# Kernel tuning notes

Measured on AMD Instinct MI355X. Metric: run time of the kernel, lower is better.

The kernel has to match this reference:

```python
import jax, jax.numpy as jnp
import numpy as np

N, DM, F, G, FG = 4096, 512, 128, 8, 16
DH, DE, ES = 128, 256, 4
E = G * ES
GROUP_TOP_K, EXPERT_TOP_K = 2, 2
TEMP = 1.0
LN_EPS = 1e-5


def _ln(x, g, b):
    m = jnp.mean(x, axis=-1, keepdims=True)
    v = jnp.mean((x - m) ** 2, axis=-1, keepdims=True)
    return (x - m) * jax.lax.rsqrt(v + LN_EPS) * g + b


def _topk_softmax(logits, k):
    # faithful to torch _topk_softmax: softmax over top-k values, zeros elsewhere
    vals, idx = jax.lax.top_k(logits, k)
    w = jax.nn.softmax(vals, axis=-1)
    oh = jax.nn.one_hot(idx, logits.shape[-1], dtype=logits.dtype)  # [..., k, E]
    return jnp.einsum('...ke,...k->...e', oh, w)


def setup_inputs() -> dict:
    key = jax.random.key(0)
    ks = iter(jax.random.split(key, 32))
    n = lambda shape, s=0.02: jax.random.normal(next(ks), shape, dtype=jnp.float32) * s
    d = {
        'hidden': jax.random.normal(next(ks), (N, DM), dtype=jnp.float32),
        'feat': jax.random.normal(next(ks), (N, F), dtype=jnp.float32),
        # pre_ln
        'pre_ln_g': jnp.ones((DM,), jnp.float32), 'pre_ln_b': jnp.zeros((DM,), jnp.float32),
        # router_hidden_encoder: LN(DM) -> Lin(DM,DH) -> GELU -> Lin(DH,DH)
        'rh_ln_g': jnp.ones((DM,), jnp.float32), 'rh_ln_b': jnp.zeros((DM,), jnp.float32),
        'rh_w1': n((DM, DH)), 'rh_b1': jnp.zeros((DH,), jnp.float32),
        'rh_w2': n((DH, DH)), 'rh_b2': jnp.zeros((DH,), jnp.float32),
        # stage_feature_encoder: LN(F) -> Lin(F,DH) -> GELU -> Lin(DH,DH)
        'sf_ln_g': jnp.ones((F,), jnp.float32), 'sf_ln_b': jnp.zeros((F,), jnp.float32),
        'sf_w1': n((F, DH)), 'sf_b1': jnp.zeros((DH,), jnp.float32),
        'sf_w2': n((DH, DH)), 'sf_b2': jnp.zeros((DH,), jnp.float32),
        # group_feature_encoders (stacked over G): LN(FG) -> Lin(FG,DH) -> GELU -> Lin(DH,DH)
        'gf_ln_g': jnp.ones((G, FG), jnp.float32), 'gf_ln_b': jnp.zeros((G, FG), jnp.float32),
        'gf_w1': n((G, FG, DH)), 'gf_b1': jnp.zeros((G, DH), jnp.float32),
        'gf_w2': n((G, DH, DH)), 'gf_b2': jnp.zeros((G, DH), jnp.float32),
        # per_group_scorer (ScalarRouter): Lin(4DH,DH) -> GELU -> Lin(DH,1)
        'pgs_w1': n((4 * DH, DH)), 'pgs_b1': jnp.zeros((DH,), jnp.float32),
        'pgs_w2': n((DH,)), 'pgs_b2': jnp.zeros((), jnp.float32),
        # intra_routers (stacked over G): Lin(4DH,DH) -> GELU -> Lin(DH,ES)
        'ir_w1': n((G, 4 * DH, DH)), 'ir_b1': jnp.zeros((G, DH), jnp.float32),
        'ir_w2': n((G, DH, ES)), 'ir_b2': jnp.zeros((G, ES), jnp.float32),
        # experts (stacked over E = G*ES, group-major): Lin(DM,DE) -> GELU -> Lin(DE,DM)
        'ex_w1': n((E, DM, DE)), 'ex_b1': jnp.zeros((E, DE), jnp.float32),
        'ex_w2': n((E, DE, DM)), 'ex_b2': jnp.zeros((E, DM), jnp.float32),
    }
    return d


def reference(hidden, feat, pre_ln_g, pre_ln_b, rh_ln_g, rh_ln_b, rh_w1, rh_b1, rh_w2, rh_b2,
              sf_ln_g, sf_ln_b, sf_w1, sf_b1, sf_w2, sf_b2,
              gf_ln_g, gf_ln_b, gf_w1, gf_b1, gf_w2, gf_b2,
              pgs_w1, pgs_b1, pgs_w2, pgs_b2,
              ir_w1, ir_b1, ir_w2, ir_b2,
              ex_w1, ex_b1, ex_w2, ex_b2):
    # expert input (pre-LN hidden)
    h_norm = _ln(hidden, pre_ln_g, pre_ln_b)                         # [N, DM]

    # factorized router encoders
    h_enc = jax.nn.gelu(_ln(hidden, rh_ln_g, rh_ln_b) @ rh_w1 + rh_b1) @ rh_w2 + rh_b2   # [N, DH]
    s_enc = jax.nn.gelu(_ln(feat, sf_ln_g, sf_ln_b) @ sf_w1 + sf_b1) @ sf_w2 + sf_b2     # [N, DH]
    gfeat = feat.reshape(N, G, FG)                                    # disjoint contiguous group features
    g_h = jax.nn.gelu(jnp.einsum('ngf,gfh->ngh', _ln(gfeat, gf_ln_g, gf_ln_b), gf_w1) + gf_b1)
    g_enc = jnp.einsum('ngh,ghk->ngk', g_h, gf_w2) + gf_b2            # [N, G, DH]

    hB = jnp.broadcast_to(h_enc[:, None, :], (N, G, DH))
    sB = jnp.broadcast_to(s_enc[:, None, :], (N, G, DH))
    router_in = jnp.concatenate([hB, sB, g_enc, hB * g_enc], axis=-1)  # [N, G, 4DH]

    # per-group scalar scores -> group logits -> top-k scatter softmax
    pg_h = jax.nn.gelu(jnp.einsum('ngi,ih->ngh', router_in, pgs_w1) + pgs_b1)
    group_logits = (jnp.einsum('ngh,h->ng', pg_h, pgs_w2) + pgs_b2) / max(TEMP, 1e-6)    # [N, G]
    group_w = _topk_softmax(group_logits, GROUP_TOP_K)                 # [N, G]

    # intra-group expert routers -> top-k scatter softmax over expert_scale
    ir_h = jax.nn.gelu(jnp.einsum('ngi,gih->ngh', router_in, ir_w1) + ir_b1)
    intra_logits = jnp.einsum('ngh,ghe->nge', ir_h, ir_w2) + ir_b2     # [N, G, ES]
    intra_w = _topk_softmax(intra_logits, EXPERT_TOP_K)                # [N, G, ES]

    comb_w = (group_w[:, :, None] * intra_w).reshape(N, E)             # group-major expert order

    # per-expert GELU MLPs on pre-LN hidden (dense compute, sparse weights)
    eh = jax.nn.gelu(jnp.einsum('nd,edh->neh', h_norm, ex_w1) + ex_b1) # [N, E, DE]
    eo = jnp.einsum('neh,ehd->ned', eh, ex_w2) + ex_b2                 # [N, E, DM]
    out = jnp.einsum('ne,ned->nd', comb_w, eo)                         # [N, DM]
    return out
```

## Files before the change

### kernel.cpp

```cpp
#include <hip/hip_runtime.h>
#include <hip/hip_bf16.h>
#include <math.h>

#define N_TOK 4096
#define DM 512
#define FDIM 128
#define G 8
#define FG 16
#define DH 128
#define DE 256
#define ES 4
#define E_EXP 32
#define LN_EPS 1e-5f
#define BT 32

typedef __attribute__((ext_vector_type(8))) short bf16x8;
typedef __attribute__((ext_vector_type(4))) float f32x4;

#define MFMA16(a, b, c) __builtin_amdgcn_mfma_f32_16x16x32_bf16((a), (b), (c), 0, 0, 0)

#define PSTRIDE 6144

__device__ __forceinline__ float gelu_t(float x) {
    const float c = 0.7978845608028654f;
    float x3 = x * x * x;
    return 0.5f * x * (1.0f + tanhf(c * (x + 0.044715f * x3)));
}

__device__ __forceinline__ short f2bf(float f) {
    __hip_bfloat16 h = __float2bfloat16(f);
    return *reinterpret_cast<short*>(&h);
}
__device__ __forceinline__ float bf2f(short s) {
    __hip_bfloat16 h = *reinterpret_cast<__hip_bfloat16*>(&s);
    return __bfloat162float(h);
}
__device__ __forceinline__ void split3(float x, short& h, short& m, short& l) {
    h = f2bf(x);
    float r = x - bf2f(h);
    m = f2bf(r);
    float r2 = r - bf2f(m);
    l = f2bf(r2);
}

struct ConvJob { const float* src; short* dh; short* dm; short* dl;
                 int KB, NB, Kreal, plain, blk0; };
struct ConvJobs { ConvJob j[10]; };

__global__ void k_pre(ConvJobs J, int nconv,
                      const float* __restrict__ hidden,
                      const float* __restrict__ pg, const float* __restrict__ pb,
                      const float* __restrict__ rg, const float* __restrict__ rb,
                      __hip_bfloat16* __restrict__ h_normb, float* __restrict__ hL) {
    int b = blockIdx.x;
    if (b >= nconv) {
        int n = b - nconv;
        int j = threadIdx.x;
        const float* x = hidden + (size_t)n * DM;
        float v0 = x[j], v1 = x[j + 256];
        float s = v0 + v1, q = v0 * v0 + v1 * v1;
#pragma unroll
        for (int o = 32; o; o >>= 1) { s += __shfl_down(s, o); q += __shfl_down(q, o); }
        __shared__ float red[8];
        int w = j >> 6;
        if ((j & 63) == 0) { red[w] = s; red[4 + w] = q; }
        __syncthreads();
        float sum = red[0] + red[1] + red[2] + red[3];
        float sq  = red[4] + red[5] + red[6] + red[7];
        float m = sum * (1.0f / DM);
        float var = sq * (1.0f / DM) - m * m;
        float rs = rsqrtf(var + LN_EPS);
        float t0 = (v0 - m) * rs, t1 = (v1 - m) * rs;
        size_t base = (size_t)n * DM;
        h_normb[base + j]       = __float2bfloat16(t0 * pg[j]       + pb[j]);
        h_normb[base + j + 256] = __float2bfloat16(t1 * pg[j + 256] + pb[j + 256]);
        hL[base + j]           = t0 * rg[j]       + rb[j];
        hL[base + j + 256]     = t1 * rg[j + 256] + rb[j + 256];
        return;
    }
    int ji = 0;
#pragma unroll
    for (int i = 1; i < 10; i++) if (b >= J.j[i].blk0) ji = i;
    const ConvJob jb = J.j[ji];
    int rel = b - jb.blk0;
    int mat = rel / jb.KB, kb = rel % jb.KB;
    int ncols = jb.NB * 16;
    const float* s = jb.src + (size_t)mat * jb.Kreal * ncols;
    size_t dbase = ((size_t)mat * jb.KB + kb) * jb.NB * 512;
    for (int p = threadIdx.x; p < jb.NB * 64; p += 256) {
        int nb = p >> 6, lane = p & 63;
        int row0 = kb * 32 + ((lane >> 4) << 3);
        int col = nb * 16 + (lane & 15);
        if (jb.plain) {
            union { short sh[8]; uint4 v; } t;
#pragma unroll
            for (int j = 0; j < 8; j++) {
                float x = (row0 + j < jb.Kreal) ? s[(size_t)(row0 + j) * ncols + col] : 0.f;
                t.sh[j] = f2bf(x);
            }
            *(uint4*)&jb.dh[dbase + (size_t)p * 8] = t.v;
        } else {
            union { short sh[8]; uint4 v; } hi, mi, lo;
#pragma unroll
            for (int j = 0; j < 8; j++) {
                float x = (row0 + j < jb.Kreal) ? s[(size_t)(row0 + j) * ncols + col] : 0.f;
                split3(x, hi.sh[j], mi.sh[j], lo.sh[j]);
            }
            *(uint4*)&jb.dh[dbase + (size_t)p * 8] = hi.v;
            *(uint4*)&jb.dm[dbase + (size_t)p * 8] = mi.v;
            *(uint4*)&jb.dl[dbase + (size_t)p * 8] = lo.v;
        }
    }
}

__device__ __forceinline__ void emit_split_tiles(
        int tid, short (*Ah)[136], short (*Am)[136], short (*Al)[136],
        short* __restrict__ Yt, size_t panel0 ) {
    int lane_ = tid & 63, w = tid >> 6;
#pragma unroll
    for (int j = 0; j < 6; j++) {
        int combo = w * 6 + j;
        int split = combo >> 3;
        int rem = combo & 7; int t16 = rem >> 2, kb = rem & 3;
        const short* sp = (split == 0) ? &Ah[0][0] : (split == 1) ? &Am[0][0] : &Al[0][0];
        uint4 v = *(const uint4*)&sp[(t16 * 16 + (lane_ & 15)) * 136 + kb * 32 + (lane_ >> 4) * 8];
        *(uint4*)&Yt[((panel0 + t16) * 4 + kb) * 1536 + split * 512 + lane_ * 8] = v;
    }
}

template <int KB_TOT, bool DO_LN>
__device__ __forceinline__ void enc2_body(
        int bx, char* smem,
        const float* __restrict__ X,
        const float* __restrict__ lng, const float* __restrict__ lnb,
        const short* __restrict__ W1h, const short* __restrict__ W1m, const short* __restrict__ W1l,
        const float* __restrict__ B1,
        const short* __restrict__ W2h, const short* __restrict__ W2m, const short* __restrict__ W2l,
        const float* __restrict__ B2,
        short* __restrict__ Yt) {
    constexpr int K = KB_TOT * 32;
    const int n0 = bx * 32;
    const int tid = threadIdx.x;
    const int wave = tid >> 6, lane = tid & 63;
    const int quad = lane >> 4, lm = lane & 15;
    const int mt = wave & 1;
    const int ngb = (wave >> 1) * 4;

    short (*Ah)[136] = (short(*)[136])smem;
    short (*Am)[136] = (short(*)[136])(smem + 8704);
    short (*Al)[136] = (short(*)[136])(smem + 2 * 8704);

    f32x4 acc[4];
#pragma unroll
    for (int i = 0; i < 4; i++) acc[i] = (f32x4)(0.f);

    if (DO_LN) {
        for (int idx = tid; idx < 1024; idx += 256) {
            int row = idx >> 5, c4 = (idx & 31) * 4;
            float4 v = *(const float4*)&X[(size_t)(n0 + row) * K + c4];
            float s = v.x + v.y + v.z + v.w;
            float q = v.x * v.x + v.y * v.y + v.z * v.z + v.w * v.w;
#pragma unroll
            for (int o = 16; o; o >>= 1) { s += __shfl_xor(s, o); q += __shfl_xor(q, o); }
            float mean = s * (1.0f / 128.0f);
            float var = q * (1.0f / 128.0f) - mean * mean;
            float rs = rsqrtf(var + LN_EPS);
            float xv[4] = {(v.x - mean) * rs * lng[c4 + 0] + lnb[c4 + 0],
                           (v.y - mean) * rs * lng[c4 + 1] + lnb[c4 + 1],
                           (v.z - mean) * rs * lng[c4 + 2] + lnb[c4 + 2],
                           (v.w - mean) * rs * lng[c4 + 3] + lnb[c4 + 3]};
#pragma unroll
            for (int j = 0; j < 4; j++) {
                short h, m, l; split3(xv[j], h, m, l);
                Ah[row][c4 + j] = h; Am[row][c4 + j] = m; Al[row][c4 + j] = l;
            }
        }
        __syncthreads();
#pragma unroll
        for (int kb = 0; kb < KB_TOT; kb++) {
            bf16x8 ah = *(const bf16x8*)&Ah[mt * 16 + lm][kb * 32 + quad * 8];
            bf16x8 am = *(const bf16x8*)&Am[mt * 16 + lm][kb * 32 + quad * 8];
            bf16x8 al = *(const bf16x8*)&Al[mt * 16 + lm][kb * 32 + quad * 8];
#pragma unroll
            for (int nt = 0; nt < 4; nt++) {
                size_t bi = (((size_t)kb * 8 + ngb + nt) * 64 + lane) * 8;
                bf16x8 bh = *(const bf16x8*)&W1h[bi];
                bf16x8 bm = *(const bf16x8*)&W1m[bi];
                bf16x8 bl = *(const bf16x8*)&W1l[bi];
                acc[nt] = MFMA16(al, bh, acc[nt]);
                acc[nt] = MFMA16(am, bm, acc[nt]);
                acc[nt] = MFMA16(ah, bl, acc[nt]);
                acc[nt] = MFMA16(am, bh, acc[nt]);
                acc[nt] = MFMA16(ah, bm, acc[nt]);
                acc[nt] = MFMA16(ah, bh, acc[nt]);
            }
        }
    } else {
        for (int kb = 0; kb < KB_TOT; kb++) {
            const float* xs = X + (size_t)(n0 + mt * 16 + lm) * K + kb * 32 + quad * 8;
            float4 x0 = *(const float4*)xs, x1 = *(const float4*)(xs + 4);
            float xv[8] = {x0.x, x0.y, x0.z, x0.w, x1.x, x1.y, x1.z, x1.w};
            bf16x8 ah, am, al;
#pragma unroll
            for (int j = 0; j < 8; j++) {
                short h, m, l; split3(xv[j], h, m, l);
                ah[j] = h; am[j] = m; al[j] = l;
            }
#pragma unroll
            for (int nt = 0; nt < 4; nt++) {
                size_t bi = (((size_t)kb * 8 + ngb + nt) * 64 + lane) * 8;
                bf16x8 bh = *(const bf16x8*)&W1h[bi];
                bf16x8 bm = *(const bf16x8*)&W1m[bi];
                bf16x8 bl = *(const bf16x8*)&W1l[bi];
                acc[nt] = MFMA16(al, bh, acc[nt]);
                acc[nt] = MFMA16(am, bm, acc[nt]);
                acc[nt] = MFMA16(ah, bl, acc[nt]);
                acc[nt] = MFMA16(am, bh, acc[nt]);
                acc[nt] = MFMA16(ah, bm, acc[nt]);
                acc[nt] = MFMA16(ah, bh, acc[nt]);
            }
        }
    }
    __syncthreads();
#pragma unroll
    for (int nt = 0; nt < 4; nt++) {
        int col = (ngb + nt) * 16 + lm;
        float b1 = B1[col];
#pragma unroll
        for (int r = 0; r < 4; r++) {
            int row = mt * 16 + quad * 4 + r;
            short h, m, l; split3(gelu_t(acc[nt][r] + b1), h, m, l);
            Ah[row][col] = h; Am[row][col] = m; Al[row][col] = l;
        }
    }
    __syncthreads();
    f32x4 acc2[4];
#pragma unroll
    for (int i = 0; i < 4; i++) acc2[i] = (f32x4)(0.f);
#pragma unroll
    for (int kb = 0; kb < 4; kb++) {
        bf16x8 ah = *(const bf16x8*)&Ah[mt * 16 + lm][kb * 32 + quad * 8];
        bf16x8 am = *(const bf16x8*)&Am[mt * 16 + lm][kb * 32 + quad * 8];
        bf16x8 al = *(const bf16x8*)&Al[mt * 16 + lm][kb * 32 + quad * 8];
#pragma unroll
        for (int nt = 0; nt < 4; nt++) {
            size_t bi = (((size_t)kb * 8 + ngb + nt) * 64 + lane) * 8;
            bf16x8 bh = *(const bf16x8*)&W2h[bi];
            bf16x8 bm = *(const bf16x8*)&W2m[bi];
            bf16x8 bl = *(const bf16x8*)&W2l[bi];
            acc2[nt] = MFMA16(al, bh, acc2[nt]);
            acc2[nt] = MFMA16(am, bm, acc2[nt]);
            acc2[nt] = MFMA16(ah, bl, acc2[nt]);
            acc2[nt] = MFMA16(am, bh, acc2[nt]);
            acc2[nt] = MFMA16(ah, bm, acc2[nt]);
            acc2[nt] = MFMA16(ah, bh, acc2[nt]);
        }
    }
    __syncthreads();
#pragma unroll
    for (int nt = 0; nt < 4; nt++) {
        int col = (ngb + nt) * 16 + lm;
        float b2 = B2[col];
#pragma unroll
        for (int r = 0; r < 4; r++) {
            int row = mt * 16 + quad * 4 + r;
            short h, m, l; split3(acc2[nt][r] + b2, h, m, l);
            Ah[row][col] = h; Am[row][col] = m; Al[row][col] = l;
        }
    }
    __syncthreads();
    emit_split_tiles(tid, Ah, Am, Al, Yt, (size_t)bx * 2);
}

__device__ __forceinline__ void genc_one(
        int bx, int g, char* smem,
        const float* __restrict__ feat,
        const float* __restrict__ gln_g, const float* __restrict__ gln_b,
        const short* __restrict__ W1h, const short* __restrict__ W1m, const short* __restrict__ W1l,
        const float* __restrict__ gb1,
        const short* __restrict__ W2h, const short* __restrict__ W2m, const short* __restrict__ W2l,
        const float* __restrict__ gb2,
        short* __restrict__ Gs) {
    const int tid = threadIdx.x;
    const int wave = tid >> 6, lane = tid & 63;
    const int quad = lane >> 4, lm = lane & 15;
    const int mt = wave & 1;
    const int ngb = (wave >> 1) * 4;
    const int n0 = bx * 32;

    short (*Ah)[136] = (short(*)[136])smem;
    short (*Am)[136] = (short(*)[136])(smem + 8704);
    short (*Al)[136] = (short(*)[136])(smem + 2 * 8704);

    {
        int t = tid >> 3, sub = tid & 7;
        const float* fr = feat + (size_t)(n0 + t) * FDIM + g * FG;
        float xv[FG];
        float mean = 0.f;
#pragma unroll
        for (int i = 0; i < FG; i++) { xv[i] = fr[i]; mean += xv[i]; }
        mean *= (1.0f / FG);
        float var = 0.f;
#pragma unroll
        for (int i = 0; i < FG; i++) { float d = xv[i] - mean; var += d * d; }
        var *= (1.0f / FG);
        float rs = rsqrtf(var + LN_EPS);
#pragma unroll
        for (int j = 0; j < 2; j++) {
            int i = sub * 2 + j;
            float xn = (xv[i] - mean) * rs * gln_g[g * FG + i] + gln_b[g * FG + i];
            short h, m, l; split3(xn, h, m, l);
            Ah[t][i] = h; Am[t][i] = m; Al[t][i] = l;
            Ah[t][16 + i] = 0; Am[t][16 + i] = 0; Al[t][16 + i] = 0;
        }
    }
    __syncthreads();
    f32x4 acc[4];
#pragma unroll
    for (int i = 0; i < 4; i++) acc[i] = (f32x4)(0.f);
    {
        bf16x8 ah = *(const bf16x8*)&Ah[mt * 16 + lm][quad * 8];
        bf16x8 am = *(const bf16x8*)&Am[mt * 16 + lm][quad * 8];
        bf16x8 al = *(const bf16x8*)&Al[mt * 16 + lm][quad * 8];
#pragma unroll
        for (int nt = 0; nt < 4; nt++) {
            size_t bi = (((size_t)g * 8 + ngb + nt) * 64 + lane) * 8;
            bf16x8 bh = *(const bf16x8*)&W1h[bi];
            bf16x8 bm = *(const bf16x8*)&W1m[bi];
            bf16x8 bl = *(const bf16x8*)&W1l[bi];
            acc[nt] = MFMA16(al, bh, acc[nt]);
            acc[nt] = MFMA16(am, bm, acc[nt]);
            acc[nt] = MFMA16(ah, bl, acc[nt]);
            acc[nt] = MFMA16(am, bh, acc[nt]);
            acc[nt] = MFMA16(ah, bm, acc[nt]);
            acc[nt] = MFMA16(ah, bh, acc[nt]);
        }
    }
    __syncthreads();
#pragma unroll
    for (int nt = 0; nt < 4; nt++) {
        int col = (ngb + nt) * 16 + lm;
        float b1 = gb1[g * DH + col];
#pragma unroll
        for (int r = 0; r < 4; r++) {
            int row = mt * 16 + quad * 4 + r;
            short h, m, l; split3(gelu_t(acc[nt][r] + b1), h, m, l);
            Ah[row][col] = h; Am[row][col] = m; Al[row][col] = l;
        }
    }
    __syncthreads();
    f32x4 acc2[4];
#pragma unroll
    for (int i = 0; i < 4; i++) acc2[i] = (f32x4)(0.f);
#pragma unroll
    for (int kb = 0; kb < 4; kb++) {
        bf16x8 a2h = *(const bf16x8*)&Ah[mt * 16 + lm][kb * 32 + quad * 8];
        bf16x8 a2m = *(const bf16x8*)&Am[mt * 16 + lm][kb * 32 + quad * 8];
        bf16x8 a2l = *(const bf16x8*)&Al[mt * 16 + lm][kb * 32 + quad * 8];
#pragma unroll
        for (int nt = 0; nt < 4; nt++) {
            size_t bi = ((((size_t)g * 4 + kb) * 8 + ngb + nt) * 64 + lane) * 8;
            bf16x8 bh = *(const bf16x8*)&W2h[bi];
            bf16x8 bm = *(const bf16x8*)&W2m[bi];
            bf16x8 bl = *(const bf16x8*)&W2l[bi];
            acc2[nt] = MFMA16(a2l, bh, acc2[nt]);
            acc2[nt] = MFMA16(a2m, bm, acc2[nt]);
            acc2[nt] = MFMA16(a2h, bl, acc2[nt]);
            acc2[nt] = MFMA16(a2m, bh, acc2[nt]);
            acc2[nt] = MFMA16(a2h, bm, acc2[nt]);
            acc2[nt] = MFMA16(a2h, bh, acc2[nt]);
        }
    }
    __syncthreads();
#pragma unroll
    for (int nt = 0; nt < 4; nt++) {
        int col = (ngb + nt) * 16 + lm;
        float b2 = gb2[g * DH + col];
#pragma unroll
        for (int r = 0; r < 4; r++) {
            int row = mt * 16 + quad * 4 + r;
            short h, m, l; split3(acc2[nt][r] + b2, h, m, l);
            Ah[row][col] = h; Am[row][col] = m; Al[row][col] = l;
        }
    }
    __syncthreads();
    emit_split_tiles(tid, Ah, Am, Al, Gs, (size_t)g * 256 + bx * 2);
}

__global__ __launch_bounds__(256) void k_enc_all(
        const float* __restrict__ hL, const float* __restrict__ feat,
        const float* __restrict__ sf_g, const float* __restrict__ sf_b,
        const float* __restrict__ gln_g, const float* __restrict__ gln_b,
        const short* Brh1H, const short* Brh1M, const short* Brh1L, const float* rh_b1,
        const short* Brh2H, const short* Brh2M, const short* Brh2L, const float* rh_b2,
        const short* Bsf1H, const short* Bsf1M, const short* Bsf1L, const float* sf_b1,
        const short* Bsf2H, const short* Bsf2M, const short* Bsf2L, const float* sf_b2,
        const short* Bgf1H, const short* Bgf1M, const short* Bgf1L, const float* gf_b1,
        const short* Bgf2H, const short* Bgf2M, const short* Bgf2L, const float* gf_b2,
        short* __restrict__ Hs, short* __restrict__ Ss, short* __restrict__ Gs) {
    __shared__ __align__(16) char smem[3 * 8704];
    int bid = blockIdx.x;
    if (bid < 128)
        enc2_body<16, false>(bid, smem, hL, nullptr, nullptr,
                             Brh1H, Brh1M, Brh1L, rh_b1, Brh2H, Brh2M, Brh2L, rh_b2, Hs);
    else if (bid < 256)
        enc2_body<4, true>(bid - 128, smem, feat, sf_g, sf_b,
                           Bsf1H, Bsf1M, Bsf1L, sf_b1, Bsf2H, Bsf2M, Bsf2L, sf_b2, Ss);
    else {
        int idx = bid - 256;
        genc_one(idx >> 3, idx & 7, smem, feat, gln_g, gln_b,
                 Bgf1H, Bgf1M, Bgf1L, gf_b1, Bgf2H, Bgf2M, Bgf2L, gf_b2, Gs);
    }
}

__global__ __launch_bounds__(512) void k_router_mfma(
        const short* __restrict__ Hs, const short* __restrict__ Ss, const short* __restrict__ Gs,
        const short* __restrict__ BpgH, const short* __restrict__ BpgM, const short* __restrict__ BpgL,
        const short* __restrict__ BirH, const short* __restrict__ BirM, const short* __restrict__ BirL,
        const float* __restrict__ pb1, const float* __restrict__ pw2, const float* __restrict__ pb2,
        const float* __restrict__ ib1, const float* __restrict__ iw2, const float* __restrict__ ib2,
        float* __restrict__ glog, float* __restrict__ ilog) {
    const int g = blockIdx.x & 7;
    const int bx = blockIdx.x >> 3;
    const int n0 = bx * 64;
    const int tid = threadIdx.x;
    const int wave = tid >> 6, lane = tid & 63;
    const int quad = lane >> 4, lm = lane & 15;
    const bool is_pg = wave < 4;
    const int nbase = (wave & 3) * 2;
    const short* Bh = is_pg ? BpgH : (BirH + (size_t)g * 65536);
    const short* Bm = is_pg ? BpgM : (BirM + (size_t)g * 65536);
    const short* Bl = is_pg ? BpgL : (BirL + (size_t)g * 65536);

    const short* HsB = Hs + (size_t)bx * 4 * PSTRIDE;
    const short* SsB = Ss + (size_t)bx * 4 * PSTRIDE;
    const short* GsB = Gs + ((size_t)g * 256 + bx * 4) * PSTRIDE;

    __shared__ __align__(16) char smem[49152];

    int goff[6];
#pragma unroll
    for (int it = 0; it < 6; it++) {
        int lin = it * 512 + tid;
        int split = lin >> 10, rem = lin & 1023;
        int kbl = rem >> 8, t16 = (rem >> 6) & 3, ln = rem & 63;
        goff[it] = t16 * PSTRIDE + kbl * 1536 + split * 512 + ln * 8;
    }
    int roff0, roff1, woff0, woff1;
    {
        int slot = tid;
        int kbl = slot >> 8, t16 = (slot >> 6) & 3, ln = slot & 63;
        roff0 = t16 * PSTRIDE + kbl * 1536 + ln * 8;
        woff0 = kbl * 4096 + t16 * 1024 + ln * 16;
        slot = 512 + tid;
        kbl = slot >> 8; t16 = (slot >> 6) & 3; ln = slot & 63;
        roff1 = t16 * PSTRIDE + kbl * 1536 + ln * 8;
        woff1 = kbl * 4096 + t16 * 1024 + ln * 16;
    }

    f32x4 acc[4][2];
#pragma unroll
    for (int mt = 0; mt < 4; mt++)
#pragma unroll
        for (int nt = 0; nt < 2; nt++) acc[mt][nt] = (f32x4)(0.f);

    bf16x8 R[6];

#define LOADR(basep) { _Pragma("unroll") \
    for (int it = 0; it < 6; it++) R[it] = *(const bf16x8*)((basep) + goff[it]); }
#define STAGE_WRITE() { _Pragma("unroll") \
    for (int it = 0; it < 6; it++) *(bf16x8*)(smem + ((it * 512 + tid) * 16)) = R[it]; }
#define COMPUTE_CHUNK(CH) { _Pragma("unroll") \
    for (int kbl = 0; kbl < 4; kbl++) { \
        const int kb = (CH) * 4 + kbl; \
        bf16x8 Ahf[4], Amf[4], Alf[4]; \
        _Pragma("unroll") \
        for (int mt = 0; mt < 4; mt++) { \
            size_t loff = (size_t)kbl * 4096 + mt * 1024 + (size_t)lane * 16; \
            Ahf[mt] = *(const bf16x8*)(smem + loff); \
            Amf[mt] = *(const bf16x8*)(smem + 16384 + loff); \
            Alf[mt] = *(const bf16x8*)(smem + 32768 + loff); \
        } \
        _Pragma("unroll") \
        for (int nt = 0; nt < 2; nt++) { \
            size_t bi = (((size_t)kb * 8 + nbase + nt) * 64 + lane) * 8; \
            bf16x8 bh = *(const bf16x8*)&Bh[bi]; \
            bf16x8 bm = *(const bf16x8*)&Bm[bi]; \
            bf16x8 bl = *(const bf16x8*)&Bl[bi]; \
            _Pragma("unroll") \
            for (int mt = 0; mt < 4; mt++) { \
                acc[mt][nt] = MFMA16(Alf[mt], bh, acc[mt][nt]); \
                acc[mt][nt] = MFMA16(Amf[mt], bm, acc[mt][nt]); \
                acc[mt][nt] = MFMA16(Ahf[mt], bl, acc[mt][nt]); \
                acc[mt][nt] = MFMA16(Amf[mt], bh, acc[mt][nt]); \
                acc[mt][nt] = MFMA16(Ahf[mt], bm, acc[mt][nt]); \
                acc[mt][nt] = MFMA16(Ahf[mt], bh, acc[mt][nt]); \
            } \
        } \
    } }

    LOADR(HsB);
    STAGE_WRITE();
    __syncthreads();
    LOADR(SsB);
    COMPUTE_CHUNK(0);

    __syncthreads();
    STAGE_WRITE();
    __syncthreads();
    LOADR(GsB);
    COMPUTE_CHUNK(1);

    __syncthreads();
    STAGE_WRITE();
    __syncthreads();
    bf16x8 Hv0_0 = *(const bf16x8*)(HsB + roff0);
    bf16x8 Hv0_1 = *(const bf16x8*)(HsB + roff0 + 512);
    bf16x8 Hv0_2 = *(const bf16x8*)(HsB + roff0 + 1024);
    bf16x8 Gv0_0 = *(const bf16x8*)(GsB + roff0);
    bf16x8 Gv0_1 = *(const bf16x8*)(GsB + roff0 + 512);
    bf16x8 Gv0_2 = *(const bf16x8*)(GsB + roff0 + 1024);
    bf16x8 Hv1_0 = *(const bf16x8*)(HsB + roff1);
    bf16x8 Hv1_1 = *(const bf16x8*)(HsB + roff1 + 512);
    bf16x8 Hv1_2 = *(const bf16x8*)(HsB + roff1 + 1024);
    bf16x8 Gv1_0 = *(const bf16x8*)(GsB + roff1);
    bf16x8 Gv1_1 = *(const bf16x8*)(GsB + roff1 + 512);
    bf16x8 Gv1_2 = *(const bf16x8*)(GsB + roff1 + 1024);
    COMPUTE_CHUNK(2);

    bf16x8 P0h, P0m, P0l, P1h, P1m, P1l;
#pragma unroll
    for (int j = 0; j < 8; j++) {
        float hv = bf2f(Hv0_0[j]) + bf2f(Hv0_1[j]) + bf2f(Hv0_2[j]);
        float gv = bf2f(Gv0_0[j]) + bf2f(Gv0_1[j]) + bf2f(Gv0_2[j]);
        short a_, b_, c_; split3(hv * gv, a_, b_, c_);
        P0h[j] = a_; P0m[j] = b_; P0l[j] = c_;
    }
#pragma unroll
    for (int j = 0; j < 8; j++) {
        float hv = bf2f(Hv1_0[j]) + bf2f(Hv1_1[j]) + bf2f(Hv1_2[j]);
        float gv = bf2f(Gv1_0[j]) + bf2f(Gv1_1[j]) + bf2f(Gv1_2[j]);
        short a_, b_, c_; split3(hv * gv, a_, b_, c_);
        P1h[j] = a_; P1m[j] = b_; P1l[j] = c_;
    }

    __syncthreads();
    *(bf16x8*)(smem + woff0)         = P0h;
    *(bf16x8*)(smem + 16384 + woff0) = P0m;
    *(bf16x8*)(smem + 32768 + woff0) = P0l;
    *(bf16x8*)(smem + woff1)         = P1h;
    *(bf16x8*)(smem + 16384 + woff1) = P1m;
    *(bf16x8*)(smem + 32768 + woff1) = P1l;
    __syncthreads();
    COMPUTE_CHUNK(3);

#undef LOADR
#undef STAGE_WRITE
#undef COMPUTE_CHUNK

    float (*ph)[129] = (float(*)[129])smem;
    float (*ih)[129] = (float(*)[129])(smem + 32 * 129 * 4);
    for (int h = 0; h < 2; h++) {
        __syncthreads();
#pragma unroll
        for (int mi = 0; mi < 2; mi++) {
            int mt = 2 * h + mi;
#pragma unroll
            for (int nt = 0; nt < 2; nt++) {
                int col = (nbase + nt) * 16 + lm;
                float b1 = is_pg ? pb1[col] : ib1[g * DH + col];
                float* dst = is_pg ? &ph[0][0] : &ih[0][0];
#pragma unroll
                for (int r = 0; r < 4; r++) {
                    int row = mi * 16 + quad * 4 + r;
                    dst[row * 129 + col] = gelu_t(acc[mt][nt][r] + b1);
                }
            }
        }
        __syncthreads();
        if (tid < 128) {
            int t = tid >> 2, q = tid & 3;
            float s = 0.f;
            for (int i = q * 32; i < q * 32 + 32; i++) s += ph[t][i] * pw2[i];
            s += __shfl_xor(s, 1);
            s += __shfl_xor(s, 2);
            if (q == 0) glog[(size_t)(n0 + h * 32 + t) * G + g] = s + pb2[0];
        } else if (tid < 384) {
            int t2 = tid - 128;
            int t = t2 >> 3, e = (t2 >> 1) & 3, half = t2 & 1;
            const float* wv = iw2 + (size_t)g * DH * ES;
            float s = 0.f;
            for (int i = half * 64; i < half * 64 + 64; i++) s += ih[t][i] * wv[i * ES + e];
            s += __shfl_xor(s, 1);
            if (half == 0) ilog[((size_t)(n0 + h * 32 + t) * G + g) * ES + e] = s + ib2[g * ES + e];
        }
    }
}

__global__ void k_topk(const float* __restrict__ glog, const float* __restrict__ ilog,
                       int* __restrict__ cnt, int* __restrict__ toks, float* __restrict__ wgts) {
    int n = blockIdx.x * blockDim.x + threadIdx.x;
    if (n >= N_TOK) return;
    float gl[G];
#pragma unroll
    for (int g = 0; g < G; g++) gl[g] = glog[(size_t)n * G + g];
    int i1 = 0; float v1 = gl[0];
#pragma unroll
    for (int g = 1; g < G; g++) if (gl[g] > v1) { v1 = gl[g]; i1 = g; }
    int i2 = -1; float v2 = -1e30f;
#pragma unroll
    for (int g = 0; g < G; g++) if (g != i1 && gl[g] > v2) { v2 = gl[g]; i2 = g; }
    float eg = expf(v2 - v1);
    float den = 1.0f / (1.0f + eg);
    float gw_sel[2] = { den, eg * den };
    int g_sel[2] = { i1, i2 };
#pragma unroll
    for (int s = 0; s < 2; s++) {
        int g = g_sel[s]; float gw = gw_sel[s];
        float il[ES];
#pragma unroll
        for (int e = 0; e < ES; e++) il[e] = ilog[((size_t)n * G + g) * ES + e];
        int j1 = 0; float u1 = il[0];
#pragma unroll
        for (int e = 1; e < ES; e++) if (il[e] > u1) { u1 = il[e]; j1 = e; }
        int j2 = -1; float u2 = -1e30f;
#pragma unroll
        for (int e = 0; e < ES; e++) if (e != j1 && il[e] > u2) { u2 = il[e]; j2 = e; }
        float ei = expf(u2 - u1);
        float d2 = 1.0f / (1.0f + ei);
        int ex1 = g * ES + j1, ex2 = g * ES + j2;
        int p1 = atomicAdd(&cnt[ex1], 1);
        toks[(size_t)ex1 * N_TOK + p1] = n * 4 + s * 2;     wgts[(size_t)ex1 * N_TOK + p1] = gw * d2;
        int p2 = atomicAdd(&cnt[ex2], 1);
        toks[(size_t)ex2 * N_TOK + p2] = n * 4 + s * 2 + 1; wgts[(size_t)ex2 * N_TOK + p2] = gw * ei * d2;
    }
}

__global__ __launch_bounds__(512) void k_expert_mfma(
        const __hip_bfloat16* __restrict__ h_normb,
        const short* __restrict__ wB1, const float* __restrict__ eb1,
        const short* __restrict__ wB2, const float* __restrict__ eb2,
        const int* __restrict__ cnt, const int* __restrict__ toks,
        const float* __restrict__ wgts, float* __restrict__ part) {
    const int e = blockIdx.x & 31;
    const int slot = blockIdx.x >> 5;
    const int c = cnt[e];
    const int start = slot * BT;
    if (start >= c) return;
    const int m = min(BT, c - start);

    __shared__ short hs[BT][520];
    short (*es)[264] = (short(*)[264])&hs[0][0];
    __shared__ int   tok_s[BT];
    __shared__ float w_s[BT];

    const int tid = threadIdx.x;
    if (tid < BT) {
        bool ok = tid < m;
        tok_s[tid] = ok ? toks[(size_t)e * N_TOK + start + tid] : 0;
        w_s[tid]   = ok ? wgts[(size_t)e * N_TOK + start + tid] : 0.f;
    }
    __syncthreads();
    for (int idx = tid; idx < BT * 64; idx += 512) {
        int t = idx >> 6, ch = idx & 63;
        uint4 v = make_uint4(0, 0, 0, 0);
        if (t < m) v = *((const uint4*)(h_normb + (size_t)(tok_s[t] >> 2) * DM) + ch);
        *(uint4*)&hs[t][ch * 8] = v;
    }
    __syncthreads();

    const int wave = tid >> 6, lane = tid & 63;
    const int quad = lane >> 4, lm = lane & 15;

    const int ng = wave * 2;
    f32x4 acc1[2][2];
#pragma unroll
    for (int a = 0; a < 2; a++)
#pragma unroll
        for (int b = 0; b < 2; b++) acc1[a][b] = (f32x4)(0.f);
    {
        const short* w1e = wB1 + (size_t)e * DM * DE;
        for (int kb = 0; kb < 16; kb++) {
            bf16x8 a0 = *(const bf16x8*)&hs[lm][kb * 32 + quad * 8];
            bf16x8 a1 = *(const bf16x8*)&hs[16 + lm][kb * 32 + quad * 8];
            const short* wp = w1e + ((size_t)kb * 16 + ng) * 512 + lane * 8;
#pragma unroll
            for (int nt = 0; nt < 2; nt++) {
                bf16x8 b = *(const bf16x8*)(wp + nt * 512);
                acc1[0][nt] = MFMA16(a0, b, acc1[0][nt]);
                acc1[1][nt] = MFMA16(a1, b, acc1[1][nt]);
            }
        }
    }
    __syncthreads();
#pragma unroll
    for (int nt = 0; nt < 2; nt++) {
        int col = (ng + nt) * 16 + lm;
        float b1 = eb1[e * DE + col];
#pragma unroll
        for (int mt = 0; mt < 2; mt++)
#pragma unroll
        for (int r = 0; r < 4; r++) {
            int row = mt * 16 + quad * 4 + r;
            es[row][col] = f2bf(gelu_t(acc1[mt][nt][r] + b1));
        }
    }
    __syncthreads();

    {
        const int ng2 = wave * 4;
        f32x4 acc[2][4];
#pragma unroll
        for (int a = 0; a < 2; a++)
#pragma unroll
            for (int b = 0; b < 4; b++) acc[a][b] = (f32x4)(0.f);
        const short* w2e = wB2 + (size_t)e * DE * DM;
        for (int kb = 0; kb < 8; kb++) {
            bf16x8 a0 = *(const bf16x8*)&es[lm][kb * 32 + quad * 8];
            bf16x8 a1 = *(const bf16x8*)&es[16 + lm][kb * 32 + quad * 8];
            const short* wp = w2e + ((size_t)kb * 32 + ng2) * 512 + lane * 8;
#pragma unroll
            for (int nt = 0; nt < 4; nt++) {
                bf16x8 b = *(const bf16x8*)(wp + nt * 512);
                acc[0][nt] = MFMA16(a0, b, acc[0][nt]);
                acc[1][nt] = MFMA16(a1, b, acc[1][nt]);
            }
        }
        const float* b2 = eb2 + (size_t)e * DM;
#pragma unroll
        for (int mt = 0; mt < 2; mt++)
#pragma unroll
        for (int r = 0; r < 4; r++) {
            int row = mt * 16 + quad * 4 + r;
            if (row < m) {
                float w = w_s[row];
                float* prow = part + (size_t)tok_s[row] * DM;
#pragma unroll
                for (int nt = 0; nt < 4; nt++) {
                    int col = (ng2 + nt) * 16 + lm;
                    prow[col] = w * (acc[mt][nt][r] + b2[col]);
                }
            }
        }
    }
}

__global__ void k_reduce(const float* __restrict__ part, float* __restrict__ out) {
    int n = blockIdx.x;
    int j = threadIdx.x;
    const float4* p = (const float4*)(part + (size_t)n * 4 * DM);
    float4 a = p[j], b = p[128 + j], c = p[256 + j], d = p[384 + j];
    float4 r = make_float4(a.x + b.x + c.x + d.x, a.y + b.y + c.y + d.y,
                           a.z + b.z + c.z + d.z, a.w + b.w + c.w + d.w);
    ((float4*)(out + (size_t)n * DM))[j] = r;
}

extern "C" void kernel_launch(void* const* d_in, const int* in_sizes, int n_in,
                              void* d_out, int out_size, void* d_ws, size_t ws_size,
                              hipStream_t stream) {
    const float* hidden  = (const float*)d_in[0];
    const float* feat    = (const float*)d_in[1];
    const float* pre_g   = (const float*)d_in[2];
    const float* pre_b   = (const float*)d_in[3];
    const float* rh_g    = (const float*)d_in[4];
    const float* rh_b    = (const float*)d_in[5];
    const float* rh_w1   = (const float*)d_in[6];
    const float* rh_b1   = (const float*)d_in[7];
    const float* rh_w2   = (const float*)d_in[8];
    const float* rh_b2   = (const float*)d_in[9];
    const float* sf_g    = (const float*)d_in[10];
    const float* sf_b    = (const float*)d_in[11];
    const float* sf_w1   = (const float*)d_in[12];
    const float* sf_b1   = (const float*)d_in[13];
    const float* sf_w2   = (const float*)d_in[14];
    const float* sf_b2   = (const float*)d_in[15];
    const float* gln_g   = (const float*)d_in[16];
    const float* gln_b   = (const float*)d_in[17];
    const float* gf_w1   = (const float*)d_in[18];
    const float* gf_b1   = (const float*)d_in[19];
    const float* gf_w2   = (const float*)d_in[20];
    const float* gf_b2   = (const float*)d_in[21];
    const float* pgs_w1  = (const float*)d_in[22];
    const float* pgs_b1  = (const float*)d_in[23];
    const float* pgs_w2  = (const float*)d_in[24];
    const float* pgs_b2  = (const float*)d_in[25];
    const float* ir_w1   = (const float*)d_in[26];
    const float* ir_b1   = (const float*)d_in[27];
    const float* ir_w2   = (const float*)d_in[28];
    const float* ir_b2   = (const float*)d_in[29];
    const float* ex_w1   = (const float*)d_in[30];
    const float* ex_b1   = (const float*)d_in[31];
    const float* ex_w2   = (const float*)d_in[32];
    const float* ex_b2   = (const float*)d_in[33];
    float* out = (float*)d_out;

    char* w = (char*)d_ws;
    auto alloc = [&](size_t bytes) { void* r = (void*)w; w += (bytes + 255) & ~(size_t)255; return r; };
    __hip_bfloat16* h_normb = (__hip_bfloat16*)alloc((size_t)N_TOK * DM * 2);
    short* Hs    = (short*)alloc((size_t)256 * PSTRIDE * 2);
    short* Ss    = (short*)alloc((size_t)256 * PSTRIDE * 2);
    float* glog  = (float*)alloc((size_t)N_TOK * G * 4);
    float* ilog  = (float*)alloc((size_t)N_TOK * G * ES * 4);
    float* wgts  = (float*)alloc((size_t)E_EXP * N_TOK * 4);
    short* wB1   = (short*)alloc((size_t)E_EXP * DM * DE * 2);
    short* wB2   = (short*)alloc((size_t)E_EXP * DE * DM * 2);
    short* BpgH  = (short*)alloc((size_t)16 * 8 * 512 * 2);
    short* BpgM  = (short*)alloc((size_t)16 * 8 * 512 * 2);
    short* BpgL  = (short*)alloc((size_t)16 * 8 * 512 * 2);
    short* BirH  = (short*)alloc((size_t)G * 16 * 8 * 512 * 2);
    short* BirM  = (short*)alloc((size_t)G * 16 * 8 * 512 * 2);
    short* BirL  = (short*)alloc((size_t)G * 16 * 8 * 512 * 2);
    short* Brh1H = (short*)alloc((size_t)16 * 8 * 512 * 2);
    short* Brh1M = (short*)alloc((size_t)16 * 8 * 512 * 2);
    short* Brh1L = (short*)alloc((size_t)16 * 8 * 512 * 2);
    short* Brh2H = (short*)alloc((size_t)4 * 8 * 512 * 2);
    short* Brh2M = (short*)alloc((size_t)4 * 8 * 512 * 2);
    short* Brh2L = (short*)alloc((size_t)4 * 8 * 512 * 2);
    short* Bsf1H = (short*)alloc((size_t)4 * 8 * 512 * 2);
    short* Bsf1M = (short*)alloc((size_t)4 * 8 * 512 * 2);
    short* Bsf1L = (short*)alloc((size_t)4 * 8 * 512 * 2);
    short* Bsf2H = (short*)alloc((size_t)4 * 8 * 512 * 2);
    short* Bsf2M = (short*)alloc((size_t)4 * 8 * 512 * 2);
    short* Bsf2L = (short*)alloc((size_t)4 * 8 * 512 * 2);
    short* Bgf1H = (short*)alloc((size_t)G * 1 * 8 * 512 * 2);
    short* Bgf1M = (short*)alloc((size_t)G * 1 * 8 * 512 * 2);
    short* Bgf1L = (short*)alloc((size_t)G * 1 * 8 * 512 * 2);
    short* Bgf2H = (short*)alloc((size_t)G * 4 * 8 * 512 * 2);
    short* Bgf2M = (short*)alloc((size_t)G * 4 * 8 * 512 * 2);
    short* Bgf2L = (short*)alloc((size_t)G * 4 * 8 * 512 * 2);
    int* cnt     = (int*)alloc(E_EXP * 4);
    int* toks    = (int*)alloc((size_t)E_EXP * N_TOK * 4);
    char* uni   = (char*)alloc((size_t)N_TOK * 4 * DM * 4);
    float* hL   = (float*)uni;
    short* Gs   = (short*)(uni + (size_t)N_TOK * DM * 4);
    float* part = (float*)uni;

    hipMemsetAsync(cnt, 0, E_EXP * sizeof(int), stream);

    ConvJobs J;
    int b0 = 0;
    auto mkjob = [&](int i, const float* s, short* dh, short* dm, short* dl,
                     int KB, int NB, int Kreal, int plain, int nmat) {
        J.j[i] = ConvJob{s, dh, dm, dl, KB, NB, Kreal, plain, b0};
        b0 += KB * nmat;
    };
    mkjob(0, ex_w1, wB1, nullptr, nullptr, 16, 16, 512, 1, E_EXP);
    mkjob(1, ex_w2, wB2, nullptr, nullptr, 8, 32, 256, 1, E_EXP);
    mkjob(2, pgs_w1, BpgH, BpgM, BpgL, 16, 8, 512, 0, 1);
    mkjob(3, ir_w1, BirH, BirM, BirL, 16, 8, 512, 0, G);
    mkjob(4, rh_w1, Brh1H, Brh1M, Brh1L, 16, 8, 512, 0, 1);
    mkjob(5, rh_w2, Brh2H, Brh2M, Brh2L, 4, 8, 128, 0, 1);
    mkjob(6, sf_w1, Bsf1H, Bsf1M, Bsf1L, 4, 8, 128, 0, 1);
    mkjob(7, sf_w2, Bsf2H, Bsf2M, Bsf2L, 4, 8, 128, 0, 1);
    mkjob(8, gf_w1, Bgf1H, Bgf1M, Bgf1L, 1, 8, 16, 0, G);
    mkjob(9, gf_w2, Bgf2H, Bgf2M, Bgf2L, 4, 8, 128, 0, G);
    k_pre<<<b0 + N_TOK, 256, 0, stream>>>(J, b0, hidden, pre_g, pre_b, rh_g, rh_b, h_normb, hL);

    k_enc_all<<<256 + (N_TOK / 32) * G, 256, 0, stream>>>(
        hL, feat, sf_g, sf_b, gln_g, gln_b,
        Brh1H, Brh1M, Brh1L, rh_b1, Brh2H, Brh2M, Brh2L, rh_b2,
        Bsf1H, Bsf1M, Bsf1L, sf_b1, Bsf2H, Bsf2M, Bsf2L, sf_b2,
        Bgf1H, Bgf1M, Bgf1L, gf_b1, Bgf2H, Bgf2M, Bgf2L, gf_b2,
        Hs, Ss, Gs);

    k_router_mfma<<<(N_TOK / 64) * G, 512, 0, stream>>>(Hs, Ss, Gs,
                                             BpgH, BpgM, BpgL, BirH, BirM, BirL,
                                             pgs_b1, pgs_w2, pgs_b2, ir_b1, ir_w2, ir_b2,
                                             glog, ilog);

    k_topk<<<N_TOK / 256, 256, 0, stream>>>(glog, ilog, cnt, toks, wgts);
    k_expert_mfma<<<(N_TOK / BT) * E_EXP, 512, 0, stream>>>(h_normb, wB1, ex_b1, wB2, ex_b2,
                                                            cnt, toks, wgts, part);
    k_reduce<<<N_TOK, 128, 0, stream>>>(part, out);
}
```

Measured before the change: 345.6 us.

## Store encoder outputs as fp32 and split to bf16x3 inside router kernel

The encoder kernel now writes fp32 h/s/g encodings directly instead of pre-splitting them into three bf16 tiles laid out in MFMA panel order through shared memory. The router kernel loads fp32 rows, splits them into hi/mid/lo bf16 and stages them itself. The h*g product is formed in fp32 from the staged g tile and the reloaded h row. This removes the encoder's shared-memory staging round trip and two barriers, and cuts intermediate traffic from 6 bytes to 4 bytes per element. In exchange the router does the split arithmetic and reads the h row twice.

```diff
diff --git a/kernel.cpp b/kernel.cpp
--- a/kernel.cpp
+++ b/kernel.cpp
@@ -18,8 +18,6 @@
 typedef __attribute__((ext_vector_type(4))) float f32x4;
 
 #define MFMA16(a, b, c) __builtin_amdgcn_mfma_f32_16x16x32_bf16((a), (b), (c), 0, 0, 0)
-
-#define PSTRIDE 6144
 
 __device__ __forceinline__ float gelu_t(float x) {
     const float c = 0.7978845608028654f;
@@ -113,21 +111,6 @@
     }
 }
 
-__device__ __forceinline__ void emit_split_tiles(
-        int tid, short (*Ah)[136], short (*Am)[136], short (*Al)[136],
-        short* __restrict__ Yt, size_t panel0 ) {
-    int lane_ = tid & 63, w = tid >> 6;
-#pragma unroll
-    for (int j = 0; j < 6; j++) {
-        int combo = w * 6 + j;
-        int split = combo >> 3;
-        int rem = combo & 7; int t16 = rem >> 2, kb = rem & 3;
-        const short* sp = (split == 0) ? &Ah[0][0] : (split == 1) ? &Am[0][0] : &Al[0][0];
-        uint4 v = *(const uint4*)&sp[(t16 * 16 + (lane_ & 15)) * 136 + kb * 32 + (lane_ >> 4) * 8];
-        *(uint4*)&Yt[((panel0 + t16) * 4 + kb) * 1536 + split * 512 + lane_ * 8] = v;
-    }
-}
-
 template <int KB_TOT, bool DO_LN>
 __device__ __forceinline__ void enc2_body(
         int bx, char* smem,
@@ -137,7 +120,7 @@
         const float* __restrict__ B1,
         const short* __restrict__ W2h, const short* __restrict__ W2m, const short* __restrict__ W2l,
         const float* __restrict__ B2,
-        short* __restrict__ Yt) {
+        float* __restrict__ Y) {
     constexpr int K = KB_TOT * 32;
     const int n0 = bx * 32;
     const int tid = threadIdx.x;
@@ -146,9 +129,9 @@
     const int mt = wave & 1;
     const int ngb = (wave >> 1) * 4;
 
-    short (*Ah)[136] = (short(*)[136])smem;
-    short (*Am)[136] = (short(*)[136])(smem + 8704);
-    short (*Al)[136] = (short(*)[136])(smem + 2 * 8704);
+    short (*Ah)[132] = (short(*)[132])smem;
+    short (*Am)[132] = (short(*)[132])(smem + 32 * 132 * 2);
+    short (*Al)[132] = (short(*)[132])(smem + 2 * 32 * 132 * 2);
 
     f32x4 acc[4];
 #pragma unroll
@@ -256,7 +239,6 @@
             acc2[nt] = MFMA16(ah, bh, acc2[nt]);
         }
     }
-    __syncthreads();
 #pragma unroll
     for (int nt = 0; nt < 4; nt++) {
         int col = (ngb + nt) * 16 + lm;
@@ -264,12 +246,9 @@
 #pragma unroll
         for (int r = 0; r < 4; r++) {
             int row = mt * 16 + quad * 4 + r;
-            short h, m, l; split3(acc2[nt][r] + b2, h, m, l);
-            Ah[row][col] = h; Am[row][col] = m; Al[row][col] = l;
-        }
-    }
-    __syncthreads();
-    emit_split_tiles(tid, Ah, Am, Al, Yt, (size_t)bx * 2);
+            Y[(size_t)(n0 + row) * DH + col] = acc2[nt][r] + b2;
+        }
+    }
 }
 
 __device__ __forceinline__ void genc_one(
@@ -280,7 +259,7 @@
         const float* __restrict__ gb1,
         const short* __restrict__ W2h, const short* __restrict__ W2m, const short* __restrict__ W2l,
         const float* __restrict__ gb2,
-        short* __restrict__ Gs) {
+        float* __restrict__ g_enc) {
     const int tid = threadIdx.x;
     const int wave = tid >> 6, lane = tid & 63;
     const int quad = lane >> 4, lm = lane & 15;
@@ -288,9 +267,9 @@
     const int ngb = (wave >> 1) * 4;
     const int n0 = bx * 32;
 
-    short (*Ah)[136] = (short(*)[136])smem;
-    short (*Am)[136] = (short(*)[136])(smem + 8704);
-    short (*Al)[136] = (short(*)[136])(smem + 2 * 8704);
+    short (*Ah)[132] = (short(*)[132])smem;
+    short (*Am)[132] = (short(*)[132])(smem + 8448);
+    short (*Al)[132] = (short(*)[132])(smem + 2 * 8448);
 
     {
         int t = tid >> 3, sub = tid & 7;
@@ -371,7 +350,6 @@
             acc2[nt] = MFMA16(a2h, bh, acc2[nt]);
         }
     }
-    __syncthreads();
 #pragma unroll
     for (int nt = 0; nt < 4; nt++) {
         int col = (ngb + nt) * 16 + lm;
@@ -379,12 +357,9 @@
 #pragma unroll
         for (int r = 0; r < 4; r++) {
             int row = mt * 16 + quad * 4 + r;
-            short h, m, l; split3(acc2[nt][r] + b2, h, m, l);
-            Ah[row][col] = h; Am[row][col] = m; Al[row][col] = l;
-        }
-    }
-    __syncthreads();
-    emit_split_tiles(tid, Ah, Am, Al, Gs, (size_t)g * 256 + bx * 2);
+            g_enc[((size_t)(n0 + row) * G + g) * DH + col] = acc2[nt][r] + b2;
+        }
+    }
 }
 
 __global__ __launch_bounds__(256) void k_enc_all(
@@ -397,24 +372,39 @@
         const short* Bsf2H, const short* Bsf2M, const short* Bsf2L, const float* sf_b2,
         const short* Bgf1H, const short* Bgf1M, const short* Bgf1L, const float* gf_b1,
         const short* Bgf2H, const short* Bgf2M, const short* Bgf2L, const float* gf_b2,
-        short* __restrict__ Hs, short* __restrict__ Ss, short* __restrict__ Gs) {
-    __shared__ __align__(16) char smem[3 * 8704];
+        float* __restrict__ h_enc, float* __restrict__ s_enc, float* __restrict__ g_enc) {
+    __shared__ __align__(16) char smem[3 * 8448];
     int bid = blockIdx.x;
     if (bid < 128)
         enc2_body<16, false>(bid, smem, hL, nullptr, nullptr,
-                             Brh1H, Brh1M, Brh1L, rh_b1, Brh2H, Brh2M, Brh2L, rh_b2, Hs);
+                             Brh1H, Brh1M, Brh1L, rh_b1, Brh2H, Brh2M, Brh2L, rh_b2, h_enc);
     else if (bid < 256)
         enc2_body<4, true>(bid - 128, smem, feat, sf_g, sf_b,
-                           Bsf1H, Bsf1M, Bsf1L, sf_b1, Bsf2H, Bsf2M, Bsf2L, sf_b2, Ss);
+                           Bsf1H, Bsf1M, Bsf1L, sf_b1, Bsf2H, Bsf2M, Bsf2L, sf_b2, s_enc);
     else {
         int idx = bid - 256;
         genc_one(idx >> 3, idx & 7, smem, feat, gln_g, gln_b,
-                 Bgf1H, Bgf1M, Bgf1L, gf_b1, Bgf2H, Bgf2M, Bgf2L, gf_b2, Gs);
-    }
+                 Bgf1H, Bgf1M, Bgf1L, gf_b1, Bgf2H, Bgf2M, Bgf2L, gf_b2, g_enc);
+    }
+}
+
+__device__ __forceinline__ void stage16v(float4 a, float4 b, float4 c, float4 d,
+                                         char* smem, int wo0, int wo1) {
+    float v0[8] = {a.x, a.y, a.z, a.w, b.x, b.y, b.z, b.w};
+    float v1[8] = {c.x, c.y, c.z, c.w, d.x, d.y, d.z, d.w};
+    bf16x8 h0, m0, l0, h1, m1, l1;
+#pragma unroll
+    for (int j = 0; j < 8; j++) { short hh, mm, ll; split3(v0[j], hh, mm, ll); h0[j]=hh; m0[j]=mm; l0[j]=ll; }
+#pragma unroll
+    for (int j = 0; j < 8; j++) { short hh, mm, ll; split3(v1[j], hh, mm, ll); h1[j]=hh; m1[j]=mm; l1[j]=ll; }
+    *(bf16x8*)(smem + wo0) = h0;           *(bf16x8*)(smem + wo1) = h1;
+    *(bf16x8*)(smem + 16384 + wo0) = m0;   *(bf16x8*)(smem + 16384 + wo1) = m1;
+    *(bf16x8*)(smem + 32768 + wo0) = l0;   *(bf16x8*)(smem + 32768 + wo1) = l1;
 }
 
 __global__ __launch_bounds__(512) void k_router_mfma(
-        const short* __restrict__ Hs, const short* __restrict__ Ss, const short* __restrict__ Gs,
+        const float* __restrict__ h_enc, const float* __restrict__ s_enc,
+        const float* __restrict__ g_enc,
         const short* __restrict__ BpgH, const short* __restrict__ BpgM, const short* __restrict__ BpgL,
         const short* __restrict__ BirH, const short* __restrict__ BirM, const short* __restrict__ BirL,
         const float* __restrict__ pb1, const float* __restrict__ pw2, const float* __restrict__ pb2,
@@ -432,31 +422,15 @@
     const short* Bm = is_pg ? BpgM : (BirM + (size_t)g * 65536);
     const short* Bl = is_pg ? BpgL : (BirL + (size_t)g * 65536);
 
-    const short* HsB = Hs + (size_t)bx * 4 * PSTRIDE;
-    const short* SsB = Ss + (size_t)bx * 4 * PSTRIDE;
-    const short* GsB = Gs + ((size_t)g * 256 + bx * 4) * PSTRIDE;
-
     __shared__ __align__(16) char smem[49152];
 
-    int goff[6];
-#pragma unroll
-    for (int it = 0; it < 6; it++) {
-        int lin = it * 512 + tid;
-        int split = lin >> 10, rem = lin & 1023;
-        int kbl = rem >> 8, t16 = (rem >> 6) & 3, ln = rem & 63;
-        goff[it] = t16 * PSTRIDE + kbl * 1536 + split * 512 + ln * 8;
-    }
-    int roff0, roff1, woff0, woff1;
-    {
-        int slot = tid;
-        int kbl = slot >> 8, t16 = (slot >> 6) & 3, ln = slot & 63;
-        roff0 = t16 * PSTRIDE + kbl * 1536 + ln * 8;
-        woff0 = kbl * 4096 + t16 * 1024 + ln * 16;
-        slot = 512 + tid;
-        kbl = slot >> 8; t16 = (slot >> 6) & 3; ln = slot & 63;
-        roff1 = t16 * PSTRIDE + kbl * 1536 + ln * 8;
-        woff1 = kbl * 4096 + t16 * 1024 + ln * 16;
-    }
+    const int sr = tid >> 3, scb = tid & 7;
+    const float* hrow = h_enc + (size_t)(n0 + sr) * DH + scb * 16;
+    const float* srow = s_enc + (size_t)(n0 + sr) * DH + scb * 16;
+    const float* grow = g_enc + ((size_t)(n0 + sr) * G + g) * DH + scb * 16;
+    const int skbl = scb >> 1, st16 = sr >> 4, slm = sr & 15, sq0 = (scb & 1) * 2;
+    const int wo0 = skbl * 4096 + st16 * 1024 + (sq0 * 16 + slm) * 16;
+    const int wo1 = wo0 + 256;
 
     f32x4 acc[4][2];
 #pragma unroll
@@ -464,12 +438,10 @@
 #pragma unroll
         for (int nt = 0; nt < 2; nt++) acc[mt][nt] = (f32x4)(0.f);
 
-    bf16x8 R[6];
-
-#define LOADR(basep) { _Pragma("unroll") \
-    for (int it = 0; it < 6; it++) R[it] = *(const bf16x8*)((basep) + goff[it]); }
-#define STAGE_WRITE() { _Pragma("unroll") \
-    for (int it = 0; it < 6; it++) *(bf16x8*)(smem + ((it * 512 + tid) * 16)) = R[it]; }
+    float4 A0, A1, A2, A3;
+
+#define LOAD4(P) { const float4* p4_ = (const float4*)(P); \
+                   A0 = p4_[0]; A1 = p4_[1]; A2 = p4_[2]; A3 = p4_[3]; }
 #define COMPUTE_CHUNK(CH) { _Pragma("unroll") \
     for (int kbl = 0; kbl < 4; kbl++) { \
         const int kb = (CH) * 4 + kbl; \
@@ -499,63 +471,45 @@
         } \
     } }
 
-    LOADR(HsB);
-    STAGE_WRITE();
-    __syncthreads();
-    LOADR(SsB);
+    LOAD4(hrow);
+    stage16v(A0, A1, A2, A3, smem, wo0, wo1);
+    __syncthreads();
+    LOAD4(srow);
     COMPUTE_CHUNK(0);
 
     __syncthreads();
-    STAGE_WRITE();
-    __syncthreads();
-    LOADR(GsB);
+    stage16v(A0, A1, A2, A3, smem, wo0, wo1);
+    __syncthreads();
+    LOAD4(grow);
     COMPUTE_CHUNK(1);
 
     __syncthreads();
-    STAGE_WRITE();
-    __syncthreads();
-    bf16x8 Hv0_0 = *(const bf16x8*)(HsB + roff0);
-    bf16x8 Hv0_1 = *(const bf16x8*)(HsB + roff0 + 512);
-    bf16x8 Hv0_2 = *(const bf16x8*)(HsB + roff0 + 1024);
-    bf16x8 Gv0_0 = *(const bf16x8*)(GsB + roff0);
-    bf16x8 Gv0_1 = *(const bf16x8*)(GsB + roff0 + 512);
-    bf16x8 Gv0_2 = *(const bf16x8*)(GsB + roff0 + 1024);
-    bf16x8 Hv1_0 = *(const bf16x8*)(HsB + roff1);
-    bf16x8 Hv1_1 = *(const bf16x8*)(HsB + roff1 + 512);
-    bf16x8 Hv1_2 = *(const bf16x8*)(HsB + roff1 + 1024);
-    bf16x8 Gv1_0 = *(const bf16x8*)(GsB + roff1);
-    bf16x8 Gv1_1 = *(const bf16x8*)(GsB + roff1 + 512);
-    bf16x8 Gv1_2 = *(const bf16x8*)(GsB + roff1 + 1024);
+    stage16v(A0, A1, A2, A3, smem, wo0, wo1);
+    __syncthreads();
+    float4 H0, H1, H2, H3;
+    { const float4* p4_ = (const float4*)hrow; H0 = p4_[0]; H1 = p4_[1]; H2 = p4_[2]; H3 = p4_[3]; }
     COMPUTE_CHUNK(2);
 
-    bf16x8 P0h, P0m, P0l, P1h, P1m, P1l;
-#pragma unroll
-    for (int j = 0; j < 8; j++) {
-        float hv = bf2f(Hv0_0[j]) + bf2f(Hv0_1[j]) + bf2f(Hv0_2[j]);
-        float gv = bf2f(Gv0_0[j]) + bf2f(Gv0_1[j]) + bf2f(Gv0_2[j]);
-        short a_, b_, c_; split3(hv * gv, a_, b_, c_);
-        P0h[j] = a_; P0m[j] = b_; P0l[j] = c_;
-    }
-#pragma unroll
-    for (int j = 0; j < 8; j++) {
-        float hv = bf2f(Hv1_0[j]) + bf2f(Hv1_1[j]) + bf2f(Hv1_2[j]);
-        float gv = bf2f(Gv1_0[j]) + bf2f(Gv1_1[j]) + bf2f(Gv1_2[j]);
-        short a_, b_, c_; split3(hv * gv, a_, b_, c_);
-        P1h[j] = a_; P1m[j] = b_; P1l[j] = c_;
-    }
-
-    __syncthreads();
-    *(bf16x8*)(smem + woff0)         = P0h;
-    *(bf16x8*)(smem + 16384 + woff0) = P0m;
-    *(bf16x8*)(smem + 32768 + woff0) = P0l;
-    *(bf16x8*)(smem + woff1)         = P1h;
-    *(bf16x8*)(smem + 16384 + woff1) = P1m;
-    *(bf16x8*)(smem + 32768 + woff1) = P1l;
+    __syncthreads();
+    {
+        bf16x8 gh0 = *(const bf16x8*)(smem + wo0),          gh1 = *(const bf16x8*)(smem + wo1);
+        bf16x8 gm0 = *(const bf16x8*)(smem + 16384 + wo0),  gm1 = *(const bf16x8*)(smem + 16384 + wo1);
+        bf16x8 gl0 = *(const bf16x8*)(smem + 32768 + wo0),  gl1 = *(const bf16x8*)(smem + 32768 + wo1);
+        float gv[16];
+#pragma unroll
+        for (int j = 0; j < 8; j++) gv[j]     = bf2f(gh0[j]) + bf2f(gm0[j]) + bf2f(gl0[j]);
+#pragma unroll
+        for (int j = 0; j < 8; j++) gv[8 + j] = bf2f(gh1[j]) + bf2f(gm1[j]) + bf2f(gl1[j]);
+        float4 P0 = make_float4(H0.x * gv[0],  H0.y * gv[1],  H0.z * gv[2],  H0.w * gv[3]);
+        float4 P1 = make_float4(H1.x * gv[4],  H1.y * gv[5],  H1.z * gv[6],  H1.w * gv[7]);
+        float4 P2 = make_float4(H2.x * gv[8],  H2.y * gv[9],  H2.z * gv[10], H2.w * gv[11]);
+        float4 P3 = make_float4(H3.x * gv[12], H3.y * gv[13], H3.z * gv[14], H3.w * gv[15]);
+        stage16v(P0, P1, P2, P3, smem, wo0, wo1);
+    }
     __syncthreads();
     COMPUTE_CHUNK(3);
 
-#undef LOADR
-#undef STAGE_WRITE
+#undef LOAD4
 #undef COMPUTE_CHUNK
 
     float (*ph)[129] = (float(*)[129])smem;
@@ -797,8 +751,9 @@
     char* w = (char*)d_ws;
     auto alloc = [&](size_t bytes) { void* r = (void*)w; w += (bytes + 255) & ~(size_t)255; return r; };
     __hip_bfloat16* h_normb = (__hip_bfloat16*)alloc((size_t)N_TOK * DM * 2);
-    short* Hs    = (short*)alloc((size_t)256 * PSTRIDE * 2);
-    short* Ss    = (short*)alloc((size_t)256 * PSTRIDE * 2);
+    float* h_enc = (float*)alloc((size_t)N_TOK * DH * 4);
+    float* s_enc = (float*)alloc((size_t)N_TOK * DH * 4);
+    float* g_enc = (float*)alloc((size_t)N_TOK * G * DH * 4);
     float* glog  = (float*)alloc((size_t)N_TOK * G * 4);
     float* ilog  = (float*)alloc((size_t)N_TOK * G * ES * 4);
     float* wgts  = (float*)alloc((size_t)E_EXP * N_TOK * 4);
@@ -832,7 +787,6 @@
     int* toks    = (int*)alloc((size_t)E_EXP * N_TOK * 4);
     char* uni   = (char*)alloc((size_t)N_TOK * 4 * DM * 4);
     float* hL   = (float*)uni;
-    short* Gs   = (short*)(uni + (size_t)N_TOK * DM * 4);
     float* part = (float*)uni;
 
     hipMemsetAsync(cnt, 0, E_EXP * sizeof(int), stream);
@@ -861,9 +815,9 @@
         Brh1H, Brh1M, Brh1L, rh_b1, Brh2H, Brh2M, Brh2L, rh_b2,
         Bsf1H, Bsf1M, Bsf1L, sf_b1, Bsf2H, Bsf2M, Bsf2L, sf_b2,
         Bgf1H, Bgf1M, Bgf1L, gf_b1, Bgf2H, Bgf2M, Bgf2L, gf_b2,
-        Hs, Ss, Gs);
-
-    k_router_mfma<<<(N_TOK / 64) * G, 512, 0, stream>>>(Hs, Ss, Gs,
+        h_enc, s_enc, g_enc);
+
+    k_router_mfma<<<(N_TOK / 64) * G, 512, 0, stream>>>(h_enc, s_enc, g_enc,
                                              BpgH, BpgM, BpgL, BirH, BirM, BirL,
                                              pgs_b1, pgs_w2, pgs_b2, ir_b1, ir_w2, ir_b2,
                                              glog, ilog);
```

Result: faster. 336.2 us (-2.7%).
